# Optimization experiments

Measured on AMD Instinct MI355X. Metric: run time of the kernel, lower is better.

## Reference

```python
import jax, jax.numpy as jnp
import numpy as np


def setup_inputs() -> dict:
    key = jax.random.key(0)
    ks = jax.random.split(key, 9)
    B, H = 8192, 1024
    scale = 1.0 / np.sqrt(4 * H)
    return {
        "h": jax.random.normal(ks[0], (B, H), jnp.float32),
        "x": jax.random.normal(ks[1], (B, 2 * H), jnp.float32),
        "glo": jax.random.normal(ks[2], (B, H), jnp.float32),
        "Wi_w": jax.random.normal(ks[3], (H, 4 * H), jnp.float32) * scale,
        "Wi_b": jnp.zeros((H,), jnp.float32),
        "Wf_w": jax.random.normal(ks[4], (H, 4 * H), jnp.float32) * scale,
        "Wf_b": jnp.zeros((H,), jnp.float32),
        "Wc_w": jax.random.normal(ks[5], (H, 4 * H), jnp.float32) * scale,
        "Wc_b": jnp.zeros((H,), jnp.float32),
    }


def reference(h, x, glo, Wi_w, Wi_b, Wf_w, Wf_b, Wc_w, Wc_b):
    # Dropout is identity in eval mode (deterministic reference).
    cat_all = jnp.concatenate([h, x, glo], axis=-1)  # [B, 4H]
    # Fused gate GEMM: stack the three weight matrices, one matmul.
    W = jnp.concatenate([Wi_w, Wf_w, Wc_w], axis=0)      # [3H, 4H]
    b = jnp.concatenate([Wi_b, Wf_b, Wc_b], axis=0)      # [3H]
    gates = cat_all @ W.T + b                             # [B, 3H]
    H = h.shape[-1]
    i = jax.nn.sigmoid(gates[:, :H])
    f = jax.nn.sigmoid(gates[:, H:2 * H])
    c = jnp.tanh(gates[:, 2 * H:])
    # 2-way softmax over (i, f): alpha0 = exp(i)/(exp(i)+exp(f)) = sigmoid(i-f)
    alpha0 = jax.nn.sigmoid(i - f)
    output = alpha0 * c + (1.0 - alpha0) * h
    return output
```

## Files before the change

### kernel.cpp

```cpp
#include <hip/hip_runtime.h>

typedef unsigned short USHORT;
typedef short bf16x8 __attribute__((ext_vector_type(8)));
typedef float f32x4 __attribute__((ext_vector_type(4)));

__device__ __forceinline__ USHORT f2bf(float f) {
    unsigned u = __float_as_uint(f);
    u += 0x7fffu + ((u >> 16) & 1u);
    return (USHORT)(u >> 16);
}
__device__ __forceinline__ float bf2f(USHORT s) {
    return __uint_as_float(((unsigned)s) << 16);
}
__device__ __forceinline__ float sigm(float v) { return 1.f / (1.f + __expf(-v)); }
__device__ __forceinline__ float mytanh(float v) { return 1.f - 2.f / (__expf(2.f * v) + 1.f); }

using gcu32p = const unsigned int __attribute__((address_space(1))) *;
using lu32p  = unsigned int __attribute__((address_space(3))) *;
using lusp   = const USHORT __attribute__((address_space(3))) *;

__device__ __forceinline__ void load_lds16(const void* g, void* l) {
    __builtin_amdgcn_global_load_lds((gcu32p)g, (lu32p)l, 16, 0, 0);
}

__device__ __forceinline__ bf16x8 ds_read16(const USHORT* p) {
    bf16x8 r;
    unsigned a = (unsigned)(unsigned long long)(lusp)p;
    asm volatile("ds_read_b128 %0, %1" : "=v"(r) : "v"(a));
    return r;
}

__global__ __launch_bounds__(256) void conv_all(const float* __restrict__ h,
                                                const float* __restrict__ x,
                                                const float* __restrict__ glo,
                                                const float* __restrict__ Wi,
                                                const float* __restrict__ Wf,
                                                const float* __restrict__ Wc,
                                                USHORT* __restrict__ A,
                                                USHORT* __restrict__ W) {
    int bid = blockIdx.x;
    const float* s;
    USHORT* dst;
    int idx;
    if (bid < 8192) {
        idx = (bid * 256 + threadIdx.x) * 16;
        int m = idx >> 12, k = idx & 4095;
        if (k < 1024)      s = h   + (size_t)m * 1024 + k;
        else if (k < 3072) s = x   + (size_t)m * 2048 + (k - 1024);
        else               s = glo + (size_t)m * 1024 + (k - 3072);
        dst = A + idx;
    } else {
        idx = ((bid - 8192) * 256 + threadIdx.x) * 16;
        int n = idx >> 12, k = idx & 4095;
        const float* base = (n < 1024) ? Wi : (n < 2048 ? Wf : Wc);
        s = base + (size_t)(n & 1023) * 4096 + k;
        dst = W + idx;
    }
    float4 f0 = ((const float4*)s)[0];
    float4 f1 = ((const float4*)s)[1];
    float4 f2 = ((const float4*)s)[2];
    float4 f3 = ((const float4*)s)[3];
    union { USHORT us[16]; uint4 v[2]; } u;
    u.us[0]  = f2bf(f0.x); u.us[1]  = f2bf(f0.y); u.us[2]  = f2bf(f0.z); u.us[3]  = f2bf(f0.w);
    u.us[4]  = f2bf(f1.x); u.us[5]  = f2bf(f1.y); u.us[6]  = f2bf(f1.z); u.us[7]  = f2bf(f1.w);
    u.us[8]  = f2bf(f2.x); u.us[9]  = f2bf(f2.y); u.us[10] = f2bf(f2.z); u.us[11] = f2bf(f2.w);
    u.us[12] = f2bf(f3.x); u.us[13] = f2bf(f3.y); u.us[14] = f2bf(f3.z); u.us[15] = f2bf(f3.w);
    ((uint4*)dst)[0] = u.v[0];
    ((uint4*)dst)[1] = u.v[1];
}


#define A_ELEMS 16384
#define B_ELEMS 12288

template<int ISS, int WMODE>
__device__ __forceinline__ void do_tile(const USHORT* aRd, const USHORT* bRd,
                                        USHORT* aWr, USHORT* bWr,
                                        const USHORT* (&aG)[4], const USHORT* (&bG)[3],
                                        int koff0, f32x4 (&acc)[8][3]) {
    bf16x8 bv[3][2];
    #pragma unroll
    for (int q = 0; q < 4; ++q) {
        __builtin_amdgcn_sched_barrier(0);
        bf16x8 av[2][2];
        #pragma unroll
        for (int m2 = 0; m2 < 2; ++m2)
            #pragma unroll
            for (int kh = 0; kh < 2; ++kh)
                av[m2][kh] = ds_read16(aRd + (q * 32 + m2 * 16) * 64 + (koff0 ^ (kh * 32)));
        if (q == 0) {
            #pragma unroll
            for (int nt = 0; nt < 3; ++nt)
                #pragma unroll
                for (int kh = 0; kh < 2; ++kh)
                    bv[nt][kh] = ds_read16(bRd + nt * 4096 + (koff0 ^ (kh * 32)));
        }
        if (ISS) {
            if (q == 0) {
                load_lds16(aG[0], aWr);
                load_lds16(aG[1], aWr + 4096);
                aG[0] += 64; aG[1] += 64;
            } else if (q == 1) {
                load_lds16(aG[2], aWr + 8192);
                load_lds16(aG[3], aWr + 12288);
                aG[2] += 64; aG[3] += 64;
            } else if (q == 2) {
                load_lds16(bG[0], bWr);
                load_lds16(bG[1], bWr + 4096);
                bG[0] += 64; bG[1] += 64;
            } else {
                load_lds16(bG[2], bWr + 8192);
                bG[2] += 64;
            }
        }
        __builtin_amdgcn_sched_barrier(0);
        __builtin_amdgcn_s_barrier();
        asm volatile("s_waitcnt lgkmcnt(0)");
        __builtin_amdgcn_sched_barrier(0);
        __builtin_amdgcn_s_setprio(1);
        #pragma unroll
        for (int m2 = 0; m2 < 2; ++m2)
            #pragma unroll
            for (int nt = 0; nt < 3; ++nt)
                #pragma unroll
                for (int kh = 0; kh < 2; ++kh)
                    acc[q * 2 + m2][nt] = __builtin_amdgcn_mfma_f32_16x16x32_bf16(
                        av[m2][kh], bv[nt][kh], acc[q * 2 + m2][nt], 0, 0, 0);
        __builtin_amdgcn_s_setprio(0);
        __builtin_amdgcn_sched_barrier(0);
        if (q == 3) {
            if (WMODE == 0) asm volatile("s_waitcnt vmcnt(7)" ::: "memory");
            else if (WMODE == 1) asm volatile("s_waitcnt vmcnt(0)" ::: "memory");
        }
        __builtin_amdgcn_s_barrier();
    }
}

__global__ __launch_bounds__(512, 2) void gemm_fused(const USHORT* __restrict__ A,
                                                     const USHORT* __restrict__ B,
                                                     const float* __restrict__ bi,
                                                     const float* __restrict__ bfp,
                                                     const float* __restrict__ bc,
                                                     const float* __restrict__ h,
                                                     float* __restrict__ out) {
    __shared__ __align__(16) USHORT As[3 * 256 * 64];
    __shared__ __align__(16) USHORT Bs[2 * 192 * 64];

    const int tid  = threadIdx.x;
    const int lane = tid & 63, wv = tid >> 6;
    const int s  = (blockIdx.x & 7) * 64 + (blockIdx.x >> 3);
    const int m0 = (s & 31) * 256;
    const int n0 = (s >> 5) * 64;

    const int wM = wv >> 2, wN = wv & 3;
    const int lm = lane & 15;
    const int gw = lane >> 4;
    const int koff0 = ((gw ^ (lm >> 1)) & 7) * 8;
    const int wvOff = wv * 512;
    const int aOff = (wM * 128 + lm) * 64;
    const int bOff = (wN * 16 + lm) * 64;

    const int gswz = ((lane & 7) ^ (4 * (wv & 1) + (lane >> 4))) & 7;
    const USHORT* aG[4];
    const USHORT* bG[3];
    #pragma unroll
    for (int j = 0; j < 4; ++j)
        aG[j] = A + (size_t)(m0 + j * 64 + wv * 8 + (lane >> 3)) * 4096 + gswz * 8;
    #pragma unroll
    for (int t = 0; t < 3; ++t)
        bG[t] = B + (size_t)(t * 1024 + n0 + wv * 8 + (lane >> 3)) * 4096 + gswz * 8;

    f32x4 acc[8][3];
    #pragma unroll
    for (int a = 0; a < 8; ++a)
        #pragma unroll
        for (int b = 0; b < 3; ++b) {
            f32x4 z = {0.f, 0.f, 0.f, 0.f};
            acc[a][b] = z;
        }

    USHORT* aB0 = As;
    USHORT* aB1 = As + A_ELEMS;
    USHORT* aB2 = As + 2 * A_ELEMS;
    USHORT* bB0 = Bs;
    USHORT* bB1 = Bs + B_ELEMS;

    #pragma unroll
    for (int j = 0; j < 4; ++j) { load_lds16(aG[j], aB0 + j * 4096 + wvOff); aG[j] += 64; }
    #pragma unroll
    for (int t = 0; t < 3; ++t) { load_lds16(bG[t], bB0 + t * 4096 + wvOff); bG[t] += 64; }
    #pragma unroll
    for (int j = 0; j < 4; ++j) { load_lds16(aG[j], aB1 + j * 4096 + wvOff); aG[j] += 64; }
    #pragma unroll
    for (int t = 0; t < 3; ++t) { load_lds16(bG[t], bB1 + t * 4096 + wvOff); bG[t] += 64; }
    asm volatile("s_waitcnt vmcnt(7)" ::: "memory");
    __builtin_amdgcn_s_barrier();

    for (int kt = 0; kt < 62; ++kt) {
        do_tile<1, 0>(aB0 + aOff, bB0 + bOff, aB2 + wvOff, bB0 + wvOff,
                      aG, bG, koff0, acc);
        USHORT* tp = aB0; aB0 = aB1; aB1 = aB2; aB2 = tp;
        tp = bB0; bB0 = bB1; bB1 = tp;
    }
    do_tile<0, 1>(aB0 + aOff, bB0 + bOff, As, Bs, aG, bG, koff0, acc);
    do_tile<0, 2>(aB1 + aOff, bB1 + bOff, As, Bs, aG, bG, koff0, acc);

    const int nc = n0 + wN * 16 + lm;
    const float bbi = bi[nc], bbf = bfp[nc], bbc = bc[nc];
    #pragma unroll
    for (int mt = 0; mt < 8; ++mt) {
        #pragma unroll
        for (int r = 0; r < 4; ++r) {
            int lrow = wM * 128 + mt * 16 + (lane >> 4) * 4 + r;
            size_t off = (size_t)(m0 + lrow) * 1024 + nc;
            float gi_ = acc[mt][0][r] + bbi;
            float gf_ = acc[mt][1][r] + bbf;
            float gc_ = acc[mt][2][r] + bbc;
            float iv = sigm(gi_);
            float fv = sigm(gf_);
            float al = sigm(iv - fv);
            float cv = mytanh(gc_);
            out[off] = al * cv + (1.f - al) * h[off];
        }
    }
}

__global__ __launch_bounds__(256) void gemm3_noconv(const float* __restrict__ h,
                                                    const float* __restrict__ x,
                                                    const float* __restrict__ glo,
                                                    const float* __restrict__ Wi,
                                                    const float* __restrict__ Wf,
                                                    const float* __restrict__ Wc,
                                                    const float* __restrict__ bi,
                                                    const float* __restrict__ bfp,
                                                    const float* __restrict__ bc,
                                                    float* __restrict__ out) {
    __shared__ USHORT At[128 * 32];
    __shared__ USHORT Bt[128 * 32];
    __shared__ USHORT stash[128 * 136];

    const int tid  = threadIdx.x;
    const int lane = tid & 63, wv = tid >> 6;
    const int n0 = blockIdx.x * 128;
    const int m0 = blockIdx.y * 128;
    const int wM = wv >> 1, wN = wv & 1;
    const int lm = lane & 15, qk = (lane >> 4) * 8;
    const int rowS = tid >> 1;
    const int colS = (tid & 1) * 16;

    for (int p = 0; p < 3; ++p) {
        f32x4 acc[4][4];
        #pragma unroll
        for (int a = 0; a < 4; ++a)
            #pragma unroll
            for (int b = 0; b < 4; ++b) {
                f32x4 z = {0.f, 0.f, 0.f, 0.f};
                acc[a][b] = z;
            }
        const float* Wg = (p == 0) ? Wi : (p == 1 ? Wf : Wc);

        for (int kt = 0; kt < 128; ++kt) {
            __syncthreads();
            int k = kt * 32 + colS;
            const float* s;
            if (k < 1024)      s = h   + (size_t)(m0 + rowS) * 1024 + k;
            else if (k < 3072) s = x   + (size_t)(m0 + rowS) * 2048 + (k - 1024);
            else               s = glo + (size_t)(m0 + rowS) * 1024 + (k - 3072);
            float4 f0 = ((const float4*)s)[0], f1 = ((const float4*)s)[1];
            float4 f2 = ((const float4*)s)[2], f3 = ((const float4*)s)[3];
            union { USHORT us[8]; uint4 v; } u0, u1;
            u0.us[0]=f2bf(f0.x); u0.us[1]=f2bf(f0.y); u0.us[2]=f2bf(f0.z); u0.us[3]=f2bf(f0.w);
            u0.us[4]=f2bf(f1.x); u0.us[5]=f2bf(f1.y); u0.us[6]=f2bf(f1.z); u0.us[7]=f2bf(f1.w);
            u1.us[0]=f2bf(f2.x); u1.us[1]=f2bf(f2.y); u1.us[2]=f2bf(f2.z); u1.us[3]=f2bf(f2.w);
            u1.us[4]=f2bf(f3.x); u1.us[5]=f2bf(f3.y); u1.us[6]=f2bf(f3.z); u1.us[7]=f2bf(f3.w);
            *(uint4*)(At + rowS * 32 + colS)     = u0.v;
            *(uint4*)(At + rowS * 32 + colS + 8) = u1.v;
            const float* sw = Wg + (size_t)(n0 + rowS) * 4096 + k;
            float4 w0 = ((const float4*)sw)[0], w1 = ((const float4*)sw)[1];
            float4 w2 = ((const float4*)sw)[2], w3 = ((const float4*)sw)[3];
            union { USHORT us[8]; uint4 v; } v0, v1;
            v0.us[0]=f2bf(w0.x); v0.us[1]=f2bf(w0.y); v0.us[2]=f2bf(w0.z); v0.us[3]=f2bf(w0.w);
            v0.us[4]=f2bf(w1.x); v0.us[5]=f2bf(w1.y); v0.us[6]=f2bf(w1.z); v0.us[7]=f2bf(w1.w);
            v1.us[0]=f2bf(w2.x); v1.us[1]=f2bf(w2.y); v1.us[2]=f2bf(w2.z); v1.us[3]=f2bf(w2.w);
            v1.us[4]=f2bf(w3.x); v1.us[5]=f2bf(w3.y); v1.us[6]=f2bf(w3.z); v1.us[7]=f2bf(w3.w);
            *(uint4*)(Bt + rowS * 32 + colS)     = v0.v;
            *(uint4*)(Bt + rowS * 32 + colS + 8) = v1.v;
            __syncthreads();

            bf16x8 av[4], bv[4];
            #pragma unroll
            for (int mt = 0; mt < 4; ++mt)
                av[mt] = *(const bf16x8*)(At + (wM * 64 + mt * 16 + lm) * 32 + qk);
            #pragma unroll
            for (int nt = 0; nt < 4; ++nt)
                bv[nt] = *(const bf16x8*)(Bt + (wN * 64 + nt * 16 + lm) * 32 + qk);
            #pragma unroll
            for (int mt = 0; mt < 4; ++mt)
                #pragma unroll
                for (int nt = 0; nt < 4; ++nt)
                    acc[mt][nt] = __builtin_amdgcn_mfma_f32_16x16x32_bf16(
                        av[mt], bv[nt], acc[mt][nt], 0, 0, 0);
        }

        const float* bias = (p == 0) ? bi : (p == 1 ? bfp : bc);
        #pragma unroll
        for (int nt = 0; nt < 4; ++nt) {
            int lcol = wN * 64 + nt * 16 + lm;
            float bb = bias[n0 + lcol];
            #pragma unroll
            for (int mt = 0; mt < 4; ++mt) {
                #pragma unroll
                for (int r = 0; r < 4; ++r) {
                    int lrow = wM * 64 + mt * 16 + (lane >> 4) * 4 + r;
                    float g = acc[mt][nt][r] + bb;
                    int li = lrow * 136 + lcol;
                    if (p == 0) {
                        stash[li] = f2bf(sigm(g));
                    } else if (p == 1) {
                        float iv = bf2f(stash[li]);
                        stash[li] = f2bf(sigm(iv - sigm(g)));
                    } else {
                        float al = bf2f(stash[li]);
                        float cv = mytanh(g);
                        size_t gi = (size_t)(m0 + lrow) * 1024 + (n0 + lcol);
                        out[gi] = al * cv + (1.f - al) * h[gi];
                    }
                }
            }
        }
    }
}

extern "C" void kernel_launch(void* const* d_in, const int* in_sizes, int n_in,
                              void* d_out, int out_size, void* d_ws, size_t ws_size,
                              hipStream_t stream) {
    const float* h   = (const float*)d_in[0];
    const float* x   = (const float*)d_in[1];
    const float* glo = (const float*)d_in[2];
    const float* Wi  = (const float*)d_in[3];
    const float* bi  = (const float*)d_in[4];
    const float* Wf  = (const float*)d_in[5];
    const float* bfp = (const float*)d_in[6];
    const float* Wc  = (const float*)d_in[7];
    const float* bc  = (const float*)d_in[8];
    float* out = (float*)d_out;

    const size_t szA = (size_t)8192 * 4096 * 2;
    const size_t szW = (size_t)3072 * 4096 * 2;

    if (ws_size >= szA + szW) {
        USHORT* Abf = (USHORT*)d_ws;
        USHORT* Wbf = (USHORT*)((char*)d_ws + szA);
        conv_all<<<8192 + 3072, 256, 0, stream>>>(h, x, glo, Wi, Wf, Wc, Abf, Wbf);
        gemm_fused<<<512, 512, 0, stream>>>(Abf, Wbf, bi, bfp, bc, h, out);
    } else {
        gemm3_noconv<<<dim3(8, 64), 256, 0, stream>>>(
            h, x, glo, Wi, Wf, Wc, bi, bfp, bc, out);
    }
}
```

Before: 394.3 us.

## Restructure fused GEMM to 128x192 tiles with 4 waves and double buffering

Replaces the 256x192 block tile with 8 waves and triple-buffered A with a 128-row tile, 4 waves of 256 threads, and simple double buffering. Each k-step now issues all global-to-LDS loads up front, reads all A/B fragments, splits the MFMAs into two k-halves gated by partial lgkmcnt waits, and uses a single barrier per step instead of one per quarter. The intent is to cut barrier count and sync overhead while launching twice as many blocks. The cost is lower arithmetic intensity per block (more A/B traffic per FLOP) and a full vmcnt(0) wait each step, which reduces how much load latency is hidden.

```diff
diff --git a/kernel.cpp b/kernel.cpp
--- a/kernel.cpp
+++ b/kernel.cpp
@@ -70,105 +70,86 @@
 }
 
 
-#define A_ELEMS 16384
-#define B_ELEMS 12288
-
-template<int ISS, int WMODE>
-__device__ __forceinline__ void do_tile(const USHORT* aRd, const USHORT* bRd,
-                                        USHORT* aWr, USHORT* bWr,
-                                        const USHORT* (&aG)[4], const USHORT* (&bG)[3],
-                                        int koff0, f32x4 (&acc)[8][3]) {
-    bf16x8 bv[3][2];
-    #pragma unroll
-    for (int q = 0; q < 4; ++q) {
-        __builtin_amdgcn_sched_barrier(0);
-        bf16x8 av[2][2];
-        #pragma unroll
-        for (int m2 = 0; m2 < 2; ++m2)
-            #pragma unroll
-            for (int kh = 0; kh < 2; ++kh)
-                av[m2][kh] = ds_read16(aRd + (q * 32 + m2 * 16) * 64 + (koff0 ^ (kh * 32)));
-        if (q == 0) {
-            #pragma unroll
-            for (int nt = 0; nt < 3; ++nt)
-                #pragma unroll
-                for (int kh = 0; kh < 2; ++kh)
-                    bv[nt][kh] = ds_read16(bRd + nt * 4096 + (koff0 ^ (kh * 32)));
-        }
-        if (ISS) {
-            if (q == 0) {
-                load_lds16(aG[0], aWr);
-                load_lds16(aG[1], aWr + 4096);
-                aG[0] += 64; aG[1] += 64;
-            } else if (q == 1) {
-                load_lds16(aG[2], aWr + 8192);
-                load_lds16(aG[3], aWr + 12288);
-                aG[2] += 64; aG[3] += 64;
-            } else if (q == 2) {
-                load_lds16(bG[0], bWr);
-                load_lds16(bG[1], bWr + 4096);
-                bG[0] += 64; bG[1] += 64;
-            } else {
-                load_lds16(bG[2], bWr + 8192);
-                bG[2] += 64;
-            }
-        }
-        __builtin_amdgcn_sched_barrier(0);
-        __builtin_amdgcn_s_barrier();
-        asm volatile("s_waitcnt lgkmcnt(0)");
-        __builtin_amdgcn_sched_barrier(0);
-        __builtin_amdgcn_s_setprio(1);
-        #pragma unroll
-        for (int m2 = 0; m2 < 2; ++m2)
-            #pragma unroll
-            for (int nt = 0; nt < 3; ++nt)
-                #pragma unroll
-                for (int kh = 0; kh < 2; ++kh)
-                    acc[q * 2 + m2][nt] = __builtin_amdgcn_mfma_f32_16x16x32_bf16(
-                        av[m2][kh], bv[nt][kh], acc[q * 2 + m2][nt], 0, 0, 0);
-        __builtin_amdgcn_s_setprio(0);
-        __builtin_amdgcn_sched_barrier(0);
-        if (q == 3) {
-            if (WMODE == 0) asm volatile("s_waitcnt vmcnt(7)" ::: "memory");
-            else if (WMODE == 1) asm volatile("s_waitcnt vmcnt(0)" ::: "memory");
-        }
-        __builtin_amdgcn_s_barrier();
-    }
-}
-
-__global__ __launch_bounds__(512, 2) void gemm_fused(const USHORT* __restrict__ A,
+#define ABUF 8192
+#define BBUF 12288
+
+template<int ISS>
+__device__ __forceinline__ void kstep(const USHORT* aRd, const USHORT* bRd,
+                                      USHORT* aWr, USHORT* bWr, int tid8,
+                                      const USHORT* (&aG)[4], const USHORT* (&bG)[6],
+                                      int koff0, f32x4 (&acc)[8][3]) {
+    __builtin_amdgcn_sched_barrier(0);
+    if (ISS) {
+        #pragma unroll
+        for (int c = 0; c < 4; ++c) { load_lds16(aG[c], aWr + c * 2048 + tid8); aG[c] += 64; }
+        #pragma unroll
+        for (int c = 0; c < 6; ++c) { load_lds16(bG[c], bWr + c * 2048 + tid8); bG[c] += 64; }
+    }
+    bf16x8 a0[8], b0[3], a1[8], b1[3];
+    #pragma unroll
+    for (int mt = 0; mt < 8; ++mt) a0[mt] = ds_read16(aRd + mt * 1024 + koff0);
+    #pragma unroll
+    for (int g = 0; g < 3; ++g)    b0[g]  = ds_read16(bRd + g * 4096 + koff0);
+    #pragma unroll
+    for (int mt = 0; mt < 8; ++mt) a1[mt] = ds_read16(aRd + mt * 1024 + (koff0 ^ 32));
+    #pragma unroll
+    for (int g = 0; g < 3; ++g)    b1[g]  = ds_read16(bRd + g * 4096 + (koff0 ^ 32));
+    asm volatile("s_waitcnt lgkmcnt(11)");
+    __builtin_amdgcn_sched_barrier(0);
+    __builtin_amdgcn_s_setprio(1);
+    #pragma unroll
+    for (int mt = 0; mt < 8; ++mt)
+        #pragma unroll
+        for (int g = 0; g < 3; ++g)
+            acc[mt][g] = __builtin_amdgcn_mfma_f32_16x16x32_bf16(
+                a0[mt], b0[g], acc[mt][g], 0, 0, 0);
+    __builtin_amdgcn_s_setprio(0);
+    __builtin_amdgcn_sched_barrier(0);
+    asm volatile("s_waitcnt lgkmcnt(0)");
+    __builtin_amdgcn_sched_barrier(0);
+    __builtin_amdgcn_s_setprio(1);
+    #pragma unroll
+    for (int mt = 0; mt < 8; ++mt)
+        #pragma unroll
+        for (int g = 0; g < 3; ++g)
+            acc[mt][g] = __builtin_amdgcn_mfma_f32_16x16x32_bf16(
+                a1[mt], b1[g], acc[mt][g], 0, 0, 0);
+    __builtin_amdgcn_s_setprio(0);
+    __builtin_amdgcn_sched_barrier(0);
+    if (ISS) asm volatile("s_waitcnt vmcnt(0)" ::: "memory");
+    __builtin_amdgcn_s_barrier();
+}
+
+__global__ __launch_bounds__(256, 2) void gemm_fused(const USHORT* __restrict__ A,
                                                      const USHORT* __restrict__ B,
                                                      const float* __restrict__ bi,
                                                      const float* __restrict__ bfp,
                                                      const float* __restrict__ bc,
                                                      const float* __restrict__ h,
                                                      float* __restrict__ out) {
-    __shared__ __align__(16) USHORT As[3 * 256 * 64];
-    __shared__ __align__(16) USHORT Bs[2 * 192 * 64];
+    __shared__ __align__(16) USHORT As[2 * ABUF];
+    __shared__ __align__(16) USHORT Bs[2 * BBUF];
 
     const int tid  = threadIdx.x;
     const int lane = tid & 63, wv = tid >> 6;
-    const int s  = (blockIdx.x & 7) * 64 + (blockIdx.x >> 3);
-    const int m0 = (s & 31) * 256;
-    const int n0 = (s >> 5) * 64;
-
-    const int wM = wv >> 2, wN = wv & 3;
+    const int s  = (blockIdx.x & 7) * 128 + (blockIdx.x >> 3);
+    const int m0 = (s & 63) * 128;
+    const int n0 = (s >> 6) * 64;
+
     const int lm = lane & 15;
     const int gw = lane >> 4;
     const int koff0 = ((gw ^ (lm >> 1)) & 7) * 8;
-    const int wvOff = wv * 512;
-    const int aOff = (wM * 128 + lm) * 64;
-    const int bOff = (wN * 16 + lm) * 64;
+    const int tid8 = tid * 8;
 
     const int gswz = ((lane & 7) ^ (4 * (wv & 1) + (lane >> 4))) & 7;
     const USHORT* aG[4];
-    const USHORT* bG[3];
-    #pragma unroll
-    for (int j = 0; j < 4; ++j)
-        aG[j] = A + (size_t)(m0 + j * 64 + wv * 8 + (lane >> 3)) * 4096 + gswz * 8;
-    #pragma unroll
-    for (int t = 0; t < 3; ++t)
-        bG[t] = B + (size_t)(t * 1024 + n0 + wv * 8 + (lane >> 3)) * 4096 + gswz * 8;
+    const USHORT* bG[6];
+    #pragma unroll
+    for (int c = 0; c < 4; ++c)
+        aG[c] = A + (size_t)(m0 + c * 32 + (tid >> 3)) * 4096 + gswz * 8;
+    #pragma unroll
+    for (int c = 0; c < 6; ++c)
+        bG[c] = B + (size_t)((c >> 1) * 1024 + n0 + (c & 1) * 32 + (tid >> 3)) * 4096 + gswz * 8;
 
     f32x4 acc[8][3];
     #pragma unroll
@@ -179,39 +160,38 @@
             acc[a][b] = z;
         }
 
-    USHORT* aB0 = As;
-    USHORT* aB1 = As + A_ELEMS;
-    USHORT* aB2 = As + 2 * A_ELEMS;
-    USHORT* bB0 = Bs;
-    USHORT* bB1 = Bs + B_ELEMS;
-
-    #pragma unroll
-    for (int j = 0; j < 4; ++j) { load_lds16(aG[j], aB0 + j * 4096 + wvOff); aG[j] += 64; }
-    #pragma unroll
-    for (int t = 0; t < 3; ++t) { load_lds16(bG[t], bB0 + t * 4096 + wvOff); bG[t] += 64; }
-    #pragma unroll
-    for (int j = 0; j < 4; ++j) { load_lds16(aG[j], aB1 + j * 4096 + wvOff); aG[j] += 64; }
-    #pragma unroll
-    for (int t = 0; t < 3; ++t) { load_lds16(bG[t], bB1 + t * 4096 + wvOff); bG[t] += 64; }
-    asm volatile("s_waitcnt vmcnt(7)" ::: "memory");
+    const int lmo = lm * 64;
+    const int bro = (wv * 16 + lm) * 64;
+    const USHORT* aRd  = As + lmo;          const USHORT* bRd  = Bs + bro;
+    const USHORT* aRdN = As + ABUF + lmo;   const USHORT* bRdN = Bs + BBUF + bro;
+    USHORT* aWr  = As + ABUF;               USHORT* bWr  = Bs + BBUF;
+    USHORT* aWrN = As;                      USHORT* bWrN = Bs;
+
+    #pragma unroll
+    for (int c = 0; c < 4; ++c) { load_lds16(aG[c], As + c * 2048 + tid8); aG[c] += 64; }
+    #pragma unroll
+    for (int c = 0; c < 6; ++c) { load_lds16(bG[c], Bs + c * 2048 + tid8); bG[c] += 64; }
+    asm volatile("s_waitcnt vmcnt(0)" ::: "memory");
     __builtin_amdgcn_s_barrier();
 
-    for (int kt = 0; kt < 62; ++kt) {
-        do_tile<1, 0>(aB0 + aOff, bB0 + bOff, aB2 + wvOff, bB0 + wvOff,
-                      aG, bG, koff0, acc);
-        USHORT* tp = aB0; aB0 = aB1; aB1 = aB2; aB2 = tp;
-        tp = bB0; bB0 = bB1; bB1 = tp;
-    }
-    do_tile<0, 1>(aB0 + aOff, bB0 + bOff, As, Bs, aG, bG, koff0, acc);
-    do_tile<0, 2>(aB1 + aOff, bB1 + bOff, As, Bs, aG, bG, koff0, acc);
-
-    const int nc = n0 + wN * 16 + lm;
+    for (int kt = 0; kt < 63; ++kt) {
+        kstep<1>(aRd, bRd, aWr, bWr, tid8, aG, bG, koff0, acc);
+        const USHORT* tp;
+        tp = aRd; aRd = aRdN; aRdN = tp;
+        tp = bRd; bRd = bRdN; bRdN = tp;
+        USHORT* wp;
+        wp = aWr; aWr = aWrN; aWrN = wp;
+        wp = bWr; bWr = bWrN; bWrN = wp;
+    }
+    kstep<0>(aRd, bRd, aWr, bWr, tid8, aG, bG, koff0, acc);
+
+    const int nc = n0 + wv * 16 + lm;
     const float bbi = bi[nc], bbf = bfp[nc], bbc = bc[nc];
     #pragma unroll
     for (int mt = 0; mt < 8; ++mt) {
         #pragma unroll
         for (int r = 0; r < 4; ++r) {
-            int lrow = wM * 128 + mt * 16 + (lane >> 4) * 4 + r;
+            int lrow = mt * 16 + (lane >> 4) * 4 + r;
             size_t off = (size_t)(m0 + lrow) * 1024 + nc;
             float gi_ = acc[mt][0][r] + bbi;
             float gf_ = acc[mt][1][r] + bbf;
@@ -352,7 +332,7 @@
         USHORT* Abf = (USHORT*)d_ws;
         USHORT* Wbf = (USHORT*)((char*)d_ws + szA);
         conv_all<<<8192 + 3072, 256, 0, stream>>>(h, x, glo, Wi, Wf, Wc, Abf, Wbf);
-        gemm_fused<<<512, 512, 0, stream>>>(Abf, Wbf, bi, bfp, bc, h, out);
+        gemm_fused<<<1024, 256, 0, stream>>>(Abf, Wbf, bi, bfp, bc, h, out);
     } else {
         gemm3_noconv<<<dim3(8, 64), 256, 0, stream>>>(
             h, x, glo, Wi, Wf, Wc, bi, bfp, bc, out);
```

Measured after the change: 393.9 us. No clear change (-0.1%).
